# Optimization experiments

Hardware: AMD Instinct MI355X
Metric: run time of the kernel (lower is better)

## Reference

```python
import jax, jax.numpy as jnp
import numpy as np

EPS = 1e-5  # nn.LayerNorm default
TOP_K = 2


def setup_inputs() -> dict:
    key = jax.random.key(0)
    ks = jax.random.split(key, 8)
    B, S, D, H, E = 4, 2048, 512, 512, 8
    sd = lambda fan_in: 1.0 / np.sqrt(fan_in)
    x = jax.random.normal(ks[0], (B, S, D), dtype=jnp.float32)
    # gate: Linear(D, E, bias=False)
    Wg = jax.random.uniform(ks[1], (D, E), jnp.float32, -sd(D), sd(D))
    # stacked expert params (ExpertModule): fc1 D->H, fc2 H->D, LayerNorm(D)
    W1 = jax.random.uniform(ks[2], (E, D, H), jnp.float32, -sd(D), sd(D))
    b1 = jax.random.uniform(ks[3], (E, H), jnp.float32, -sd(D), sd(D))
    W2 = jax.random.uniform(ks[4], (E, H, D), jnp.float32, -sd(H), sd(H))
    b2 = jax.random.uniform(ks[5], (E, D), jnp.float32, -sd(H), sd(H))
    gamma = jnp.ones((E, D), jnp.float32)
    beta = jnp.zeros((E, D), jnp.float32)
    return {"x": x, "Wg": Wg, "W1": W1, "b1": b1, "W2": W2, "b2": b2,
            "gamma": gamma, "beta": beta}


def _moe_forward(x, Wg, W1, b1, W2, b2, gamma, beta):
    B, S, D = x.shape
    xf = x.reshape(-1, D)                                   # [T, D]
    # gating: top-k logits then softmax over the k selected logits only
    logits = xf @ Wg                                        # [T, E]
    topv, topi = jax.lax.top_k(logits, TOP_K)               # [T, K]
    gate_w = jax.nn.softmax(topv, axis=-1)                  # [T, K]
    # expert MLP + LayerNorm computed for all experts (dropout inactive in eval)
    h = jax.nn.relu(jnp.einsum('td,edh->teh', xf, W1) + b1[None])   # [T, E, H]
    y = jnp.einsum('teh,ehd->ted', h, W2) + b2[None]                 # [T, E, D]
    mu = jnp.mean(y, axis=-1, keepdims=True)
    var = jnp.mean((y - mu) ** 2, axis=-1, keepdims=True)
    y = (y - mu) / jnp.sqrt(var + EPS) * gamma[None] + beta[None]
    # combine: gather the k selected expert outputs and weight-sum
    y_sel = jnp.take_along_axis(y, topi[:, :, None], axis=1)        # [T, K, D]
    out = jnp.sum(gate_w[:, :, None] * y_sel, axis=1)               # [T, D]
    return out.reshape(B, S, D)


def reference(x, Wg, W1, b1, W2, b2, gamma, beta):
    return _moe_forward(x, Wg, W1, b1, W2, b2, gamma, beta)
```

## Files before the change

### kernel.cpp

```cpp
#include <hip/hip_runtime.h>
#include <hip/hip_bf16.h>


#define T_TOK   8192
#define DDIM    512
#define HDIM    512
#define NEXP    8
#define NASSIGN (T_TOK * 2)

typedef _Float16 f16x8 __attribute__((ext_vector_type(8)));
typedef _Float16 f16x4 __attribute__((ext_vector_type(4)));
typedef float    f32x4 __attribute__((ext_vector_type(4)));

__device__ __forceinline__ void gld_lds16(const _Float16* g, _Float16* l) {
    __builtin_amdgcn_global_load_lds(
        (const __attribute__((address_space(1))) unsigned int*)g,
        (__attribute__((address_space(3))) unsigned int*)l,
        16, 0, 0);
}

__global__ void transw_kernel(const float* __restrict__ W1,
                              const float* __restrict__ W2,
                              _Float16* __restrict__ W1t,
                              _Float16* __restrict__ W2t) {
    __shared__ float tile[32][33];
    int z = blockIdx.z;
    const float* src;
    _Float16* dst;
    if (z < 8) { src = W1 + (size_t)z * 512 * 512; dst = W1t + (size_t)z * 512 * 512; }
    else       { src = W2 + (size_t)(z - 8) * 512 * 512; dst = W2t + (size_t)(z - 8) * 512 * 512; }
    int bx = blockIdx.x * 32;
    int by = blockIdx.y * 32;
    int tx = threadIdx.x, ty = threadIdx.y;
#pragma unroll
    for (int i = 0; i < 4; i++) {
        int r = by + ty + i * 8;
        tile[ty + i * 8][tx] = src[(size_t)r * 512 + bx + tx];
    }
    __syncthreads();
    int tt = ty * 32 + tx;
    int row = tt >> 3;
    int jc  = tt & 7;
    f16x4 v;
#pragma unroll
    for (int k = 0; k < 4; k++) v[k] = (_Float16)tile[jc * 4 + k][row];
    *(f16x4*)(dst + (size_t)(bx + row) * 512 + by + jc * 4) = v;
}

__global__ void gate_kernel(const float* __restrict__ x,
                            const float* __restrict__ Wg,
                            _Float16* __restrict__ xh,
                            int* __restrict__ ei,
                            float* __restrict__ gw) {
    int lane = threadIdx.x & 63;
    int wave = threadIdx.x >> 6;
    int t = blockIdx.x * 4 + wave;

    const float* xr = x + (size_t)t * DDIM + lane * 8;
    float4 xa = *(const float4*)(xr);
    float4 xb = *(const float4*)(xr + 4);
    float xv[8] = {xa.x, xa.y, xa.z, xa.w, xb.x, xb.y, xb.z, xb.w};
    f16x8 hv;
#pragma unroll
    for (int j = 0; j < 8; j++) hv[j] = (_Float16)xv[j];
    *(f16x8*)(xh + (size_t)t * DDIM + lane * 8) = hv;

    double acc[NEXP];
#pragma unroll
    for (int e = 0; e < NEXP; e++) acc[e] = 0.0;
#pragma unroll
    for (int jj = 0; jj < 8; jj++) {
        int d = lane * 8 + jj;
        const float4* wr = (const float4*)(Wg + (size_t)d * NEXP);
        float4 w0 = wr[0], w1 = wr[1];
        float wv[8] = {w0.x, w0.y, w0.z, w0.w, w1.x, w1.y, w1.z, w1.w};
#pragma unroll
        for (int e = 0; e < NEXP; e++) acc[e] += (double)xv[jj] * (double)wv[e];
    }
#pragma unroll
    for (int off = 1; off < 8; off <<= 1) {
#pragma unroll
        for (int e = 0; e < NEXP; e++) acc[e] += __shfl_xor(acc[e], off, 64);
    }
    double v = acc[0];
#pragma unroll
    for (int e = 1; e < NEXP; e++) if ((lane & 7) == e) v = acc[e];
#pragma unroll
    for (int off = 8; off < 64; off <<= 1) v += __shfl_xor(v, off, 64);
    double lv[NEXP];
#pragma unroll
    for (int e = 0; e < NEXP; e++) lv[e] = __shfl(v, e, 64);

    double v0 = -1e300; int i0 = 0;
#pragma unroll
    for (int e = 0; e < NEXP; e++) if (lv[e] > v0) { v0 = lv[e]; i0 = e; }
    double v1 = -1e300; int i1 = (i0 == 0) ? 1 : 0;
#pragma unroll
    for (int e = 0; e < NEXP; e++) if (e != i0 && lv[e] > v1) { v1 = lv[e]; i1 = e; }
    if (lane == 0) {
        double ex = exp(v1 - v0);
        float g0 = (float)(1.0 / (1.0 + ex));
        float g1 = (float)(ex / (1.0 + ex));
        ei[2 * t] = i0;  ei[2 * t + 1] = i1;
        gw[2 * t] = g0;  gw[2 * t + 1] = g1;
    }
}

__global__ void count_kernel(const int* __restrict__ ei,
                             int* __restrict__ counts) {
    __shared__ int lcnt[NEXP];
    if (threadIdx.x < NEXP) lcnt[threadIdx.x] = 0;
    __syncthreads();
    int i = blockIdx.x * 512 + threadIdx.x;
    atomicAdd(&lcnt[ei[i]], 1);
    atomicAdd(&lcnt[ei[i + 256]], 1);
    __syncthreads();
    if (threadIdx.x < NEXP) atomicAdd(&counts[threadIdx.x], lcnt[threadIdx.x]);
}

__global__ void prefix_kernel(const int* __restrict__ counts,
                              int* __restrict__ offsets,
                              int* __restrict__ cursor) {
    if (threadIdx.x == 0) {
        int s = 0;
        for (int e = 0; e < NEXP; e++) { offsets[e] = s; cursor[e] = s; s += counts[e]; }
    }
}

__global__ void scatter_kernel(const int* __restrict__ ei,
                               int* __restrict__ cursor,
                               int* __restrict__ rowtok,
                               int* __restrict__ pos) {
    int t = blockIdx.x * 256 + threadIdx.x;
    int lane = threadIdx.x & 63;
#pragma unroll
    for (int k = 0; k < 2; k++) {
        int s = 2 * t + k;
        int e = ei[s];
        int r = 0;
#pragma unroll
        for (int ex = 0; ex < NEXP; ex++) {
            unsigned long long mask = __ballot(e == ex);
            if (e == ex) {
                int leader = __ffsll((unsigned long long)mask) - 1;
                int cnt = __popcll(mask);
                unsigned long long below = mask & ((lane == 63) ? 0x7fffffffffffffffull
                                                                : ((1ull << lane) - 1ull));
                int base = 0;
                if (lane == leader) base = atomicAdd(&cursor[ex], cnt);
                base = __shfl(base, leader, 64);
                r = base + __popcll(below);
            }
        }
        rowtok[r] = s;
        pos[s] = r;
    }
}

template <bool GATHER, bool RELU>
__global__ __launch_bounds__(256) void gemm_tile(
    const _Float16* __restrict__ A,
    const _Float16* __restrict__ Bt,
    const float* __restrict__ bias,
    const int* __restrict__ rowtok,
    const int* __restrict__ counts,
    const int* __restrict__ offsets,
    _Float16* __restrict__ C)
{
    int bid = blockIdx.x;
    int e = bid & 7;
    int j = bid >> 3;
    int ne = counts[e];
    int m0 = (j >> 2) * 128;
    if (m0 >= ne) return;
    int n0 = (j & 3) * 128;
    int off = offsets[e];
    const _Float16* Bte = Bt + (size_t)e * 512 * 512;

    __shared__ _Float16 As[2][128 * 32];
    __shared__ _Float16 Bs[2][128 * 32];

    int tid = threadIdx.x;
    int lane = tid & 63;
    int wave = tid >> 6;
    int wm = (wave >> 1) * 64;
    int wn = (wave & 1) * 64;
    int quad = lane >> 4;
    int l16 = lane & 15;

    int srow = tid >> 2;
    int schunk = tid & 3;

    int r0g = m0 + srow;
    int r1g = m0 + srow + 64;
    int cr0 = off + (r0g < ne ? r0g : ne - 1);
    int cr1 = off + (r1g < ne ? r1g : ne - 1);
    const _Float16* arow0;
    const _Float16* arow1;
    if (GATHER) {
        arow0 = A + (size_t)(rowtok[cr0] >> 1) * 512;
        arow1 = A + (size_t)(rowtok[cr1] >> 1) * 512;
    } else {
        arow0 = A + (size_t)cr0 * 512;
        arow1 = A + (size_t)cr1 * 512;
    }
    const _Float16* brow0 = Bte + (size_t)(n0 + srow) * 512;
    const _Float16* brow1 = Bte + (size_t)(n0 + srow + 64) * 512;

    f32x4 acc[4][4];
#pragma unroll
    for (int i = 0; i < 4; i++)
#pragma unroll
        for (int jj = 0; jj < 4; jj++) {
            acc[i][jj][0] = 0.f; acc[i][jj][1] = 0.f;
            acc[i][jj][2] = 0.f; acc[i][jj][3] = 0.f;
        }

    gld_lds16(arow0 + schunk * 8, &As[0][tid * 8]);
    gld_lds16(arow1 + schunk * 8, &As[0][tid * 8 + 64 * 32]);
    gld_lds16(brow0 + schunk * 8, &Bs[0][tid * 8]);
    gld_lds16(brow1 + schunk * 8, &Bs[0][tid * 8 + 64 * 32]);
    __syncthreads();

    int cur = 0;
    for (int t = 0; t < 16; ++t) {
        if (t < 15) {
            int k1 = (t + 1) * 32;
            gld_lds16(arow0 + k1 + schunk * 8, &As[cur ^ 1][tid * 8]);
            gld_lds16(arow1 + k1 + schunk * 8, &As[cur ^ 1][tid * 8 + 64 * 32]);
            gld_lds16(brow0 + k1 + schunk * 8, &Bs[cur ^ 1][tid * 8]);
            gld_lds16(brow1 + k1 + schunk * 8, &Bs[cur ^ 1][tid * 8 + 64 * 32]);
        }

        f16x8 af[4], bf[4];
#pragma unroll
        for (int i = 0; i < 4; i++)
            af[i] = *(const f16x8*)(&As[cur][(wm + i * 16 + l16) * 32 + quad * 8]);
#pragma unroll
        for (int jj = 0; jj < 4; jj++)
            bf[jj] = *(const f16x8*)(&Bs[cur][(wn + jj * 16 + l16) * 32 + quad * 8]);
#pragma unroll
        for (int i = 0; i < 4; i++)
#pragma unroll
            for (int jj = 0; jj < 4; jj++)
                acc[i][jj] = __builtin_amdgcn_mfma_f32_16x16x32_f16(af[i], bf[jj], acc[i][jj], 0, 0, 0);

        if (t < 15) {
            __syncthreads();
            cur ^= 1;
        }
    }

    float bcol[4];
#pragma unroll
    for (int jj = 0; jj < 4; jj++) bcol[jj] = bias[(size_t)e * 512 + n0 + wn + jj * 16 + l16];
#pragma unroll
    for (int i = 0; i < 4; i++) {
#pragma unroll
        for (int rr = 0; rr < 4; rr++) {
            int rg = m0 + wm + i * 16 + quad * 4 + rr;
            if (rg < ne) {
#pragma unroll
                for (int jj = 0; jj < 4; jj++) {
                    float v = acc[i][jj][rr] + bcol[jj];
                    if (RELU) v = fmaxf(v, 0.0f);
                    C[(size_t)(off + rg) * 512 + n0 + wn + jj * 16 + l16] = (_Float16)v;
                }
            }
        }
    }
}

__global__ void ln_combine_kernel(const _Float16* __restrict__ yb,
                                  const int* __restrict__ pos,
                                  const float* __restrict__ gw,
                                  const int* __restrict__ ei,
                                  const float* __restrict__ gamma,
                                  const float* __restrict__ beta,
                                  float* __restrict__ out) {
    int t = blockIdx.x * 4 + (threadIdx.x >> 6);
    int lane = threadIdx.x & 63;
    float o[8];
#pragma unroll
    for (int j = 0; j < 8; j++) o[j] = 0.0f;

#pragma unroll
    for (int k = 0; k < 2; k++) {
        int s = 2 * t + k;
        int r = pos[s];
        int e = ei[s];
        float w = gw[s];
        f16x8 v = *(const f16x8*)(yb + (size_t)r * 512 + lane * 8);
        float f[8];
        float sum = 0.f, sq = 0.f;
#pragma unroll
        for (int j = 0; j < 8; j++) { f[j] = (float)v[j]; sum += f[j]; sq += f[j] * f[j]; }
#pragma unroll
        for (int off = 1; off < 64; off <<= 1) {
            sum += __shfl_xor(sum, off, 64);
            sq  += __shfl_xor(sq, off, 64);
        }
        float mu = sum * (1.0f / 512.0f);
        float var = sq * (1.0f / 512.0f) - mu * mu;
        float rstd = rsqrtf(var + 1e-5f);
#pragma unroll
        for (int j = 0; j < 8; j++) {
            int d = lane * 8 + j;
            o[j] += w * ((f[j] - mu) * rstd * gamma[(size_t)e * 512 + d] + beta[(size_t)e * 512 + d]);
        }
    }
    float4* op = (float4*)(out + (size_t)t * 512 + lane * 8);
    op[0] = make_float4(o[0], o[1], o[2], o[3]);
    op[1] = make_float4(o[4], o[5], o[6], o[7]);
}

extern "C" void kernel_launch(void* const* d_in, const int* in_sizes, int n_in,
                              void* d_out, int out_size, void* d_ws, size_t ws_size,
                              hipStream_t stream) {
    const float* x     = (const float*)d_in[0];
    const float* Wg    = (const float*)d_in[1];
    const float* W1    = (const float*)d_in[2];
    const float* b1    = (const float*)d_in[3];
    const float* W2    = (const float*)d_in[4];
    const float* b2    = (const float*)d_in[5];
    const float* gamma = (const float*)d_in[6];
    const float* beta  = (const float*)d_in[7];
    float* out = (float*)d_out;

    char* w = (char*)d_ws;
    size_t o = 0;
    auto alloc = [&](size_t bytes) -> void* {
        void* p = w + o;
        o += (bytes + 255) & ~(size_t)255;
        return p;
    };
    _Float16* xh  = (_Float16*)alloc((size_t)T_TOK * DDIM * 2);
    _Float16* W1t = (_Float16*)alloc((size_t)NEXP * DDIM * HDIM * 2);
    _Float16* W2t = (_Float16*)alloc((size_t)NEXP * DDIM * HDIM * 2);
    _Float16* hb  = (_Float16*)alloc((size_t)NASSIGN * HDIM * 2);
    _Float16* yb  = (_Float16*)alloc((size_t)NASSIGN * DDIM * 2);
    float* gw     = (float*)alloc((size_t)NASSIGN * 4);
    int* ei       = (int*)alloc((size_t)NASSIGN * 4);
    int* rowtok   = (int*)alloc((size_t)NASSIGN * 4);
    int* pos      = (int*)alloc((size_t)NASSIGN * 4);
    int* counts   = (int*)alloc(NEXP * 4);
    int* offsets  = (int*)alloc(NEXP * 4);
    int* cursor   = (int*)alloc(NEXP * 4);
    (void)ws_size; (void)n_in; (void)in_sizes; (void)out_size;

    hipMemsetAsync(counts, 0, NEXP * sizeof(int), stream);

    transw_kernel<<<dim3(16, 16, 16), dim3(32, 8), 0, stream>>>(W1, W2, W1t, W2t);
    gate_kernel<<<2048, 256, 0, stream>>>(x, Wg, xh, ei, gw);
    count_kernel<<<32, 256, 0, stream>>>(ei, counts);
    prefix_kernel<<<1, 64, 0, stream>>>(counts, offsets, cursor);
    scatter_kernel<<<32, 256, 0, stream>>>(ei, cursor, rowtok, pos);

    gemm_tile<true, true><<<2048, 256, 0, stream>>>(xh, W1t, b1, rowtok, counts, offsets, hb);
    gemm_tile<false, false><<<2048, 256, 0, stream>>>(hb, W2t, b2, nullptr, counts, offsets, yb);

    ln_combine_kernel<<<2048, 256, 0, stream>>>(yb, pos, gw, ei, gamma, beta, out);
}
```

Baseline: 184.7 us.

## Fuse expert counting into gate, drop prefix kernel, swizzle GEMM LDS layout

Expert counts are now accumulated inside the gating kernel through shared-memory atomics, which removes the separate count and prefix kernels. Scatter and GEMM kernels each recompute the per-expert offsets from padded counters, and the counters are padded to avoid sharing cache lines. The GEMM tiles also XOR-swizzle the k-chunk placement in LDS to cut bank conflicts on the fragment reads. This removes two launches and an LDS bottleneck, at the cost of more global atomics from the 2048 gate blocks.

Result: no change. 184.7 us (-0.0%).

```diff
diff --git a/kernel.cpp b/kernel.cpp
--- a/kernel.cpp
+++ b/kernel.cpp
@@ -7,6 +7,7 @@
 #define HDIM    512
 #define NEXP    8
 #define NASSIGN (T_TOK * 2)
+#define CPAD    16
 
 typedef _Float16 f16x8 __attribute__((ext_vector_type(8)));
 typedef _Float16 f16x4 __attribute__((ext_vector_type(4)));
@@ -51,7 +52,12 @@
                             const float* __restrict__ Wg,
                             _Float16* __restrict__ xh,
                             int* __restrict__ ei,
-                            float* __restrict__ gw) {
+                            float* __restrict__ gw,
+                            int* __restrict__ counts) {
+    __shared__ int lcnt[NEXP];
+    if (threadIdx.x < NEXP) lcnt[threadIdx.x] = 0;
+    __syncthreads();
+
     int lane = threadIdx.x & 63;
     int wave = threadIdx.x >> 6;
     int t = blockIdx.x * 4 + wave;
@@ -103,34 +109,27 @@
         float g1 = (float)(ex / (1.0 + ex));
         ei[2 * t] = i0;  ei[2 * t + 1] = i1;
         gw[2 * t] = g0;  gw[2 * t + 1] = g1;
-    }
-}
-
-__global__ void count_kernel(const int* __restrict__ ei,
-                             int* __restrict__ counts) {
-    __shared__ int lcnt[NEXP];
-    if (threadIdx.x < NEXP) lcnt[threadIdx.x] = 0;
+        atomicAdd(&lcnt[i0], 1);
+        atomicAdd(&lcnt[i1], 1);
+    }
     __syncthreads();
-    int i = blockIdx.x * 512 + threadIdx.x;
-    atomicAdd(&lcnt[ei[i]], 1);
-    atomicAdd(&lcnt[ei[i + 256]], 1);
-    __syncthreads();
-    if (threadIdx.x < NEXP) atomicAdd(&counts[threadIdx.x], lcnt[threadIdx.x]);
-}
-
-__global__ void prefix_kernel(const int* __restrict__ counts,
-                              int* __restrict__ offsets,
-                              int* __restrict__ cursor) {
-    if (threadIdx.x == 0) {
-        int s = 0;
-        for (int e = 0; e < NEXP; e++) { offsets[e] = s; cursor[e] = s; s += counts[e]; }
+    if (threadIdx.x < NEXP) {
+        int c = lcnt[threadIdx.x];
+        if (c) atomicAdd(&counts[threadIdx.x * CPAD], c);
     }
 }
 
 __global__ void scatter_kernel(const int* __restrict__ ei,
+                               const int* __restrict__ counts,
                                int* __restrict__ cursor,
                                int* __restrict__ rowtok,
                                int* __restrict__ pos) {
+    int offs[NEXP];
+    {
+        int s = 0;
+#pragma unroll
+        for (int q = 0; q < NEXP; q++) { offs[q] = s; s += counts[q * CPAD]; }
+    }
     int t = blockIdx.x * 256 + threadIdx.x;
     int lane = threadIdx.x & 63;
 #pragma unroll
@@ -147,9 +146,9 @@
                 unsigned long long below = mask & ((lane == 63) ? 0x7fffffffffffffffull
                                                                 : ((1ull << lane) - 1ull));
                 int base = 0;
-                if (lane == leader) base = atomicAdd(&cursor[ex], cnt);
+                if (lane == leader) base = atomicAdd(&cursor[ex * CPAD], cnt);
                 base = __shfl(base, leader, 64);
-                r = base + __popcll(below);
+                r = offs[ex] + base + __popcll(below);
             }
         }
         rowtok[r] = s;
@@ -164,17 +163,24 @@
     const float* __restrict__ bias,
     const int* __restrict__ rowtok,
     const int* __restrict__ counts,
-    const int* __restrict__ offsets,
     _Float16* __restrict__ C)
 {
     int bid = blockIdx.x;
     int e = bid & 7;
     int j = bid >> 3;
-    int ne = counts[e];
+    int ne, off;
+    {
+        int s = 0; ne = 0; off = 0;
+#pragma unroll
+        for (int q = 0; q < NEXP; q++) {
+            int c = counts[q * CPAD];
+            if (q == e) { off = s; ne = c; }
+            s += c;
+        }
+    }
     int m0 = (j >> 2) * 128;
     if (m0 >= ne) return;
     int n0 = (j & 3) * 128;
-    int off = offsets[e];
     const _Float16* Bte = Bt + (size_t)e * 512 * 512;
 
     __shared__ _Float16 As[2][128 * 32];
@@ -190,6 +196,7 @@
 
     int srow = tid >> 2;
     int schunk = tid & 3;
+    int ksw = (schunk ^ ((srow >> 1) & 3)) * 8;
 
     int r0g = m0 + srow;
     int r1g = m0 + srow + 64;
@@ -216,29 +223,31 @@
             acc[i][jj][2] = 0.f; acc[i][jj][3] = 0.f;
         }
 
-    gld_lds16(arow0 + schunk * 8, &As[0][tid * 8]);
-    gld_lds16(arow1 + schunk * 8, &As[0][tid * 8 + 64 * 32]);
-    gld_lds16(brow0 + schunk * 8, &Bs[0][tid * 8]);
-    gld_lds16(brow1 + schunk * 8, &Bs[0][tid * 8 + 64 * 32]);
+    int rsw = (quad ^ ((l16 >> 1) & 3)) * 8;
+
+    gld_lds16(arow0 + ksw, &As[0][tid * 8]);
+    gld_lds16(arow1 + ksw, &As[0][tid * 8 + 64 * 32]);
+    gld_lds16(brow0 + ksw, &Bs[0][tid * 8]);
+    gld_lds16(brow1 + ksw, &Bs[0][tid * 8 + 64 * 32]);
     __syncthreads();
 
     int cur = 0;
     for (int t = 0; t < 16; ++t) {
         if (t < 15) {
             int k1 = (t + 1) * 32;
-            gld_lds16(arow0 + k1 + schunk * 8, &As[cur ^ 1][tid * 8]);
-            gld_lds16(arow1 + k1 + schunk * 8, &As[cur ^ 1][tid * 8 + 64 * 32]);
-            gld_lds16(brow0 + k1 + schunk * 8, &Bs[cur ^ 1][tid * 8]);
-            gld_lds16(brow1 + k1 + schunk * 8, &Bs[cur ^ 1][tid * 8 + 64 * 32]);
+            gld_lds16(arow0 + k1 + ksw, &As[cur ^ 1][tid * 8]);
+            gld_lds16(arow1 + k1 + ksw, &As[cur ^ 1][tid * 8 + 64 * 32]);
+            gld_lds16(brow0 + k1 + ksw, &Bs[cur ^ 1][tid * 8]);
+            gld_lds16(brow1 + k1 + ksw, &Bs[cur ^ 1][tid * 8 + 64 * 32]);
         }
 
         f16x8 af[4], bf[4];
 #pragma unroll
         for (int i = 0; i < 4; i++)
-            af[i] = *(const f16x8*)(&As[cur][(wm + i * 16 + l16) * 32 + quad * 8]);
+            af[i] = *(const f16x8*)(&As[cur][(wm + i * 16 + l16) * 32 + rsw]);
 #pragma unroll
         for (int jj = 0; jj < 4; jj++)
-            bf[jj] = *(const f16x8*)(&Bs[cur][(wn + jj * 16 + l16) * 32 + quad * 8]);
+            bf[jj] = *(const f16x8*)(&Bs[cur][(wn + jj * 16 + l16) * 32 + rsw]);
 #pragma unroll
         for (int i = 0; i < 4; i++)
 #pragma unroll
@@ -343,21 +352,18 @@
     int* ei       = (int*)alloc((size_t)NASSIGN * 4);
     int* rowtok   = (int*)alloc((size_t)NASSIGN * 4);
     int* pos      = (int*)alloc((size_t)NASSIGN * 4);
-    int* counts   = (int*)alloc(NEXP * 4);
-    int* offsets  = (int*)alloc(NEXP * 4);
-    int* cursor   = (int*)alloc(NEXP * 4);
+    int* counts   = (int*)alloc(NEXP * CPAD * 4);
+    int* cursor   = (int*)alloc(NEXP * CPAD * 4);
     (void)ws_size; (void)n_in; (void)in_sizes; (void)out_size;
 
-    hipMemsetAsync(counts, 0, NEXP * sizeof(int), stream);
+    hipMemsetAsync(counts, 0, 2 * NEXP * CPAD * sizeof(int), stream);
 
     transw_kernel<<<dim3(16, 16, 16), dim3(32, 8), 0, stream>>>(W1, W2, W1t, W2t);
-    gate_kernel<<<2048, 256, 0, stream>>>(x, Wg, xh, ei, gw);
-    count_kernel<<<32, 256, 0, stream>>>(ei, counts);
-    prefix_kernel<<<1, 64, 0, stream>>>(counts, offsets, cursor);
-    scatter_kernel<<<32, 256, 0, stream>>>(ei, cursor, rowtok, pos);
-
-    gemm_tile<true, true><<<2048, 256, 0, stream>>>(xh, W1t, b1, rowtok, counts, offsets, hb);
-    gemm_tile<false, false><<<2048, 256, 0, stream>>>(hb, W2t, b2, nullptr, counts, offsets, yb);
+    gate_kernel<<<2048, 256, 0, stream>>>(x, Wg, xh, ei, gw, counts);
+    scatter_kernel<<<32, 256, 0, stream>>>(ei, counts, cursor, rowtok, pos);
+
+    gemm_tile<true, true><<<2048, 256, 0, stream>>>(xh, W1t, b1, rowtok, counts, hb);
+    gemm_tile<false, false><<<2048, 256, 0, stream>>>(hb, W2t, b2, nullptr, counts, yb);
 
     ln_combine_kernel<<<2048, 256, 0, stream>>>(yb, pos, gw, ei, gamma, beta, out);
 }
```
